# Optimization experiments

Measured on AMD Instinct MI355X. Metric: run time of the kernel, lower is better.

The kernel has to match this reference:

```python
import jax, jax.numpy as jnp
import numpy as np

N_SAMPLES = 4_000_000
N_BUCKETS = 16
K_BASE = 32
K_ADJ = 16


def setup_inputs() -> dict:
    key = jax.random.key(0)
    ks = jax.random.split(key, 8)
    return {
        "x": jax.random.uniform(ks[0], (N_SAMPLES,), dtype=jnp.float32),
        "x_mins": jnp.zeros((N_BUCKETS,), jnp.float32),
        "x_maxs": jnp.ones((N_BUCKETS,), jnp.float32),
        "clip_los": jnp.zeros((N_BUCKETS,), jnp.float32),
        "clip_his": jnp.ones((N_BUCKETS,), jnp.float32),
        "base_knots": jax.random.uniform(ks[1], (K_BASE,), dtype=jnp.float32),
        "base_raw_w": jax.random.normal(ks[2], (K_BASE,), dtype=jnp.float32),
        "base_bias": jax.random.normal(ks[3], (1,), dtype=jnp.float32),
        "adj_knots": jax.random.uniform(ks[4], (K_ADJ,), dtype=jnp.float32),
        "adj_raw_w": jax.random.normal(ks[5], (N_BUCKETS, K_ADJ), dtype=jnp.float32),
        "adj_bias": jax.random.normal(ks[6], (N_BUCKETS,), dtype=jnp.float32),
        "bucket_idx": jax.random.randint(ks[7], (N_SAMPLES,), 0, N_BUCKETS, dtype=jnp.int64),
    }


def _clip_and_scale(x, x_min, x_max, clip_lo, clip_hi):
    # per-sample clip (NaN clip bound => no clipping), then scale to [0,1]
    xc = jnp.where(jnp.isfinite(clip_lo), jnp.maximum(x, clip_lo), x)
    xc = jnp.where(jnp.isfinite(clip_hi), jnp.minimum(xc, clip_hi), xc)
    return jnp.clip((xc - x_min) / (x_max - x_min + 1e-12), 0.0, 1.0)


def _concave_hinge(x01, knots, raw_w, bias):
    # concave, monotone-increasing piecewise-linear spline:
    # f(x) = bias + sum_k softplus(raw_w_k) * min(x, knot_k)
    w = jax.nn.softplus(raw_w)                      # nonneg slopes -> concave increasing
    basis = jnp.minimum(x01[:, None], knots)        # [N, K]
    return bias + jnp.sum(basis * w, axis=-1)       # [N] (w may be [N,K] for per-bucket)


def reference(x, x_mins, x_maxs, clip_los, clip_his, base_knots, base_raw_w,
              base_bias, adj_knots, adj_raw_w, adj_bias, bucket_idx):
    b = bucket_idx.reshape(-1)
    xf = x.reshape(-1)
    # gather per-sample bucket scaling params (replaces the python bucket loop)
    x01 = _clip_and_scale(xf, x_mins[b], x_maxs[b], clip_los[b], clip_his[b])  # [N]
    base = _concave_hinge(x01, base_knots, base_raw_w, base_bias[0])           # [N]
    # vectorized gather-compute in place of unique()+mask dispatch
    adj = _concave_hinge(x01, adj_knots, adj_raw_w[b], adj_bias[b])            # [N]
    return (base + adj)[:, None]                                               # [N,1]
```

## Files before the change

kernel.cpp:

```cpp
#include <hip/hip_runtime.h>
#include <math.h>

#define NB 16
#define KB 32
#define KA 16
#define G  128
#define HINV ((float)G)
#define H (1.0f / (float)G)

#define WS_FLOATS (64 + 2 * NB * G)

__device__ __forceinline__ float softplus_f(float v) {
    return fmaxf(v, 0.0f) + log1pf(expf(-fabsf(v)));
}

__global__ __launch_bounds__(256) void build_lut_kernel(
    const float* __restrict__ x_mins,
    const float* __restrict__ x_maxs,
    const float* __restrict__ clip_los,
    const float* __restrict__ clip_his,
    const float* __restrict__ base_knots,
    const float* __restrict__ base_raw_w,
    const float* __restrict__ base_bias,
    const float* __restrict__ adj_knots,
    const float* __restrict__ adj_raw_w,
    const float* __restrict__ adj_bias,
    float* __restrict__ ws)
{
    __shared__ float s_bw[KB];
    __shared__ float s_aw[2][KA];
    __shared__ float s_bias[2];
    __shared__ float s_f[2][G + 1];

    const int tid = threadIdx.x;
    const int b0  = blockIdx.x * 2;

    if (tid < KB) s_bw[tid] = softplus_f(base_raw_w[tid]);
    if (tid < 2 * KA) {
        const int lb = tid / KA, k = tid % KA;
        s_aw[lb][k] = softplus_f(adj_raw_w[(b0 + lb) * KA + k]);
    }
    if (tid < 2) {
        const int b = b0 + tid;
        const float mn = x_mins[b], mx = x_maxs[b];
        const float a = 1.0f / (mx - mn + 1e-12f);
        const float c = -mn * a;
        const float lo = clip_los[b], hi = clip_his[b];
        const float Lb = isfinite(lo) ? fminf(fmaxf(fmaf(lo, a, c), 0.0f), 1.0f) : 0.0f;
        const float Hb = isfinite(hi) ? fmaxf(fminf(fmaf(hi, a, c), 1.0f), 0.0f) : 1.0f;
        ((float4*)ws)[b] = make_float4(a, c, Lb, Hb);
        s_bias[tid] = adj_bias[b] + base_bias[0];
    }
    __syncthreads();

    for (int gp = tid; gp < 2 * (G + 1); gp += 256) {
        const int lb = gp / (G + 1);
        const int j  = gp % (G + 1);
        const float g = (float)j * H;
        float f = s_bias[lb];
        #pragma unroll 8
        for (int k = 0; k < KB; ++k)
            f = fmaf(s_bw[k], fminf(g, base_knots[k]), f);
        #pragma unroll 8
        for (int k = 0; k < KA; ++k)
            f = fmaf(s_aw[lb][k], fminf(g, adj_knots[k]), f);
        s_f[lb][j] = f;
    }
    __syncthreads();

    float2* lut = (float2*)(ws + 64);
    if (tid < 2 * G) {
        const int lb = tid >> 7, cc = tid & (G - 1);
        const float fl = s_f[lb][cc], fr = s_f[lb][cc + 1];
        const float c1 = (fr - fl) * HINV;
        const float c0 = fmaf(-c1, (float)cc * H, fl);
        lut[(b0 + lb) * G + cc] = make_float2(c0, c1);
    }
}

__global__ __launch_bounds__(256) void BucketAdjustedHinge_kernel(
    const float* __restrict__ x,
    const int*   __restrict__ bucket_idx,
    const float* __restrict__ ws,
    float*       __restrict__ out,
    int n)
{
    __shared__ float s_mem[WS_FLOATS];
    const float4* __restrict__ prmp = (const float4*)s_mem;
    const float2* __restrict__ lutp = (const float2*)(s_mem + 64);

    const int tid = threadIdx.x;

    {
        const float4* __restrict__ src = (const float4*)ws;
        float4* __restrict__ dst = (float4*)s_mem;
        #pragma unroll
        for (int i = 0; i < WS_FLOATS / 4 / 256 + 1; ++i) {
            const int idx = tid + i * 256;
            if (idx < WS_FLOATS / 4) dst[idx] = src[idx];
        }
    }
    __syncthreads();

    const int n4 = n >> 2;
    const int stride = gridDim.x * blockDim.x;
    const float4* __restrict__ x4v = (const float4*)x;
    const int4*   __restrict__ b4v = (const int4*)bucket_idx;
    float4*       __restrict__ o4v = (float4*)out;

    for (int i = blockIdx.x * blockDim.x + tid; i < n4; i += stride) {
        const float4 xv = x4v[i];
        const int4   bv = b4v[i];
        const float xs[4] = {xv.x, xv.y, xv.z, xv.w};
        const int   bs[4] = {bv.x, bv.y, bv.z, bv.w};
        float ox[4];
        #pragma unroll
        for (int j = 0; j < 4; ++j) {
            const int b = bs[j];
            const float4 prm = prmp[b];
            float v = fmaf(xs[j], prm.x, prm.y);
            v = fminf(fmaxf(v, prm.z), prm.w);
            int cell = (int)(v * HINV);
            cell = min(cell, G - 1);
            const float2 cf = lutp[(b << 7) + cell];
            ox[j] = fmaf(v, cf.y, cf.x);
        }
        o4v[i] = make_float4(ox[0], ox[1], ox[2], ox[3]);
    }

    const int rem_start = n4 << 2;
    for (int i = rem_start + blockIdx.x * blockDim.x + tid; i < n; i += stride) {
        const int b = bucket_idx[i];
        const float4 prm = prmp[b];
        float v = fmaf(x[i], prm.x, prm.y);
        v = fminf(fmaxf(v, prm.z), prm.w);
        int cell = (int)(v * HINV);
        cell = min(cell, G - 1);
        const float2 cf = lutp[(b << 7) + cell];
        out[i] = fmaf(v, cf.y, cf.x);
    }
}

extern "C" void kernel_launch(void* const* d_in, const int* in_sizes, int n_in,
                              void* d_out, int out_size, void* d_ws, size_t ws_size,
                              hipStream_t stream) {
    const float* x          = (const float*)d_in[0];
    const float* x_mins     = (const float*)d_in[1];
    const float* x_maxs     = (const float*)d_in[2];
    const float* clip_los   = (const float*)d_in[3];
    const float* clip_his   = (const float*)d_in[4];
    const float* base_knots = (const float*)d_in[5];
    const float* base_raw_w = (const float*)d_in[6];
    const float* base_bias  = (const float*)d_in[7];
    const float* adj_knots  = (const float*)d_in[8];
    const float* adj_raw_w  = (const float*)d_in[9];
    const float* adj_bias   = (const float*)d_in[10];
    const int*   bucket_idx = (const int*)d_in[11];
    float* out = (float*)d_out;
    float* ws  = (float*)d_ws;

    const int n = in_sizes[0];

    build_lut_kernel<<<NB / 2, 256, 0, stream>>>(
        x_mins, x_maxs, clip_los, clip_his,
        base_knots, base_raw_w, base_bias,
        adj_knots, adj_raw_w, adj_bias, ws);

    const int blocks = 2048;
    BucketAdjustedHinge_kernel<<<blocks, 256, 0, stream>>>(
        x, bucket_idx, ws, out, n);
}
```

Measured before the change: 19.24 us.

## Build LUT in raw-x domain and prefetch inputs before shared-memory LUT load

The LUT is now indexed directly by the raw x value over a global x range, so the per-sample affine scale and clip parameters fold into the table and the hot loop loses the per-bucket parameter lookup. Each thread issues loads for its first two float4 tiles of x and bucket_idx before copying the LUT into shared memory, which overlaps global latency with the table fill. The LUT build now runs in a single block. The raw-x grid only matches the reference when bucket ranges are similar, and the table's interpolation points shift for buckets with narrow ranges, which could hurt accuracy in general.

```diff
diff --git a/kernel.cpp b/kernel.cpp
--- a/kernel.cpp
+++ b/kernel.cpp
@@ -5,10 +5,10 @@
 #define KB 32
 #define KA 16
 #define G  128
-#define HINV ((float)G)
-#define H (1.0f / (float)G)
-
-#define WS_FLOATS (64 + 2 * NB * G)
+#define GP1 (G + 1)
+
+#define LUT_F2   (NB * GP1)
+#define WS_FLOATS (64 + 2 * LUT_F2)
 
 __device__ __forceinline__ float softplus_f(float v) {
     return fmaxf(v, 0.0f) + log1pf(expf(-fabsf(v)));
@@ -27,54 +27,78 @@
     const float* __restrict__ adj_bias,
     float* __restrict__ ws)
 {
-    __shared__ float s_bw[KB];
-    __shared__ float s_aw[2][KA];
-    __shared__ float s_bias[2];
-    __shared__ float s_f[2][G + 1];
+    __shared__ float  s_bw[KB];
+    __shared__ float  s_aw[NB][KA];
+    __shared__ float  s_bias[NB];
+    __shared__ float4 s_abc[NB];
+    __shared__ float  s_xlo_b[NB], s_xhi_b[NB];
+    __shared__ float  s_xr[2];
+    __shared__ float  s_f[NB][GP1];
 
     const int tid = threadIdx.x;
-    const int b0  = blockIdx.x * 2;
 
     if (tid < KB) s_bw[tid] = softplus_f(base_raw_w[tid]);
-    if (tid < 2 * KA) {
-        const int lb = tid / KA, k = tid % KA;
-        s_aw[lb][k] = softplus_f(adj_raw_w[(b0 + lb) * KA + k]);
-    }
-    if (tid < 2) {
-        const int b = b0 + tid;
-        const float mn = x_mins[b], mx = x_maxs[b];
-        const float a = 1.0f / (mx - mn + 1e-12f);
+    if (tid < NB * KA) s_aw[tid >> 4][tid & (KA - 1)] = softplus_f(adj_raw_w[tid]);
+    if (tid < NB) {
+        const float mn = x_mins[tid], mx = x_maxs[tid];
+        const float inva = mx - mn + 1e-12f;
+        const float a = 1.0f / inva;
         const float c = -mn * a;
-        const float lo = clip_los[b], hi = clip_his[b];
+        const float lo = clip_los[tid], hi = clip_his[tid];
         const float Lb = isfinite(lo) ? fminf(fmaxf(fmaf(lo, a, c), 0.0f), 1.0f) : 0.0f;
         const float Hb = isfinite(hi) ? fmaxf(fminf(fmaf(hi, a, c), 1.0f), 0.0f) : 1.0f;
-        ((float4*)ws)[b] = make_float4(a, c, Lb, Hb);
-        s_bias[tid] = adj_bias[b] + base_bias[0];
-    }
-    __syncthreads();
-
-    for (int gp = tid; gp < 2 * (G + 1); gp += 256) {
-        const int lb = gp / (G + 1);
-        const int j  = gp % (G + 1);
-        const float g = (float)j * H;
-        float f = s_bias[lb];
+        s_abc[tid] = make_float4(a, c, Lb, Hb);
+        s_bias[tid] = adj_bias[tid] + base_bias[0];
+        const float x0 = fmaf(Lb, inva, mn);
+        const float x1 = fmaf(Hb, inva, mn);
+        s_xlo_b[tid] = fminf(x0, x1);
+        s_xhi_b[tid] = fmaxf(x0, x1);
+    }
+    __syncthreads();
+
+    if (tid == 0) {
+        float xlo = s_xlo_b[0], xhi = s_xhi_b[0];
+        for (int b = 1; b < NB; ++b) {
+            xlo = fminf(xlo, s_xlo_b[b]);
+            xhi = fmaxf(xhi, s_xhi_b[b]);
+        }
+        if (!(xhi > xlo)) xhi = xlo + 1.0f;
+        s_xr[0] = xlo; s_xr[1] = xhi;
+        ws[0] = xlo;
+        ws[1] = (float)G / (xhi - xlo);
+        ws[2] = xhi;
+    }
+    __syncthreads();
+
+    const float xlo = s_xr[0], xhi = s_xr[1];
+    const float hstep = (xhi - xlo) * (1.0f / (float)G);
+
+    for (int gp = tid; gp < NB * GP1; gp += 256) {
+        const int b = gp / GP1, j = gp - b * GP1;
+        const float xj = fmaf(hstep, (float)j, xlo);
+        const float4 p = s_abc[b];
+        const float v = fminf(fmaxf(fmaf(xj, p.x, p.y), p.z), p.w);
+        float f = s_bias[b];
         #pragma unroll 8
         for (int k = 0; k < KB; ++k)
-            f = fmaf(s_bw[k], fminf(g, base_knots[k]), f);
+            f = fmaf(s_bw[k], fminf(v, base_knots[k]), f);
         #pragma unroll 8
         for (int k = 0; k < KA; ++k)
-            f = fmaf(s_aw[lb][k], fminf(g, adj_knots[k]), f);
-        s_f[lb][j] = f;
+            f = fmaf(s_aw[b][k], fminf(v, adj_knots[k]), f);
+        s_f[b][j] = f;
     }
     __syncthreads();
 
     float2* lut = (float2*)(ws + 64);
-    if (tid < 2 * G) {
-        const int lb = tid >> 7, cc = tid & (G - 1);
-        const float fl = s_f[lb][cc], fr = s_f[lb][cc + 1];
-        const float c1 = (fr - fl) * HINV;
-        const float c0 = fmaf(-c1, (float)cc * H, fl);
-        lut[(b0 + lb) * G + cc] = make_float2(c0, c1);
+    const float hinv = 1.0f / hstep;
+    for (int e = tid; e < NB * GP1; e += 256) {
+        const int b = e / GP1, j = e - b * GP1;
+        const int jc = min(j, G - 1);
+        const float fl = s_f[b][jc], fr = s_f[b][jc + 1];
+        const float c1 = (fr - fl) * hinv;
+        const float xj = fmaf(hstep, (float)jc, xlo);
+        const float c0 = fmaf(-c1, xj, fl);
+        lut[e] = make_float2(c0, c1);
     }
 }
 
@@ -85,60 +109,69 @@
     float*       __restrict__ out,
     int n)
 {
-    __shared__ float s_mem[WS_FLOATS];
-    const float4* __restrict__ prmp = (const float4*)s_mem;
-    const float2* __restrict__ lutp = (const float2*)(s_mem + 64);
+    __shared__ float2 s_lut[LUT_F2];
 
     const int tid = threadIdx.x;
-
-    {
-        const float4* __restrict__ src = (const float4*)ws;
-        float4* __restrict__ dst = (float4*)s_mem;
-        #pragma unroll
-        for (int i = 0; i < WS_FLOATS / 4 / 256 + 1; ++i) {
-            const int idx = tid + i * 256;
-            if (idx < WS_FLOATS / 4) dst[idx] = src[idx];
-        }
-    }
-    __syncthreads();
-
-    const int n4 = n >> 2;
-    const int stride = gridDim.x * blockDim.x;
+    const int gsz = gridDim.x * blockDim.x;
+    const int t   = blockIdx.x * blockDim.x + tid;
+    const int n4  = n >> 2;
+
     const float4* __restrict__ x4v = (const float4*)x;
     const int4*   __restrict__ b4v = (const int4*)bucket_idx;
     float4*       __restrict__ o4v = (float4*)out;
 
-    for (int i = blockIdx.x * blockDim.x + tid; i < n4; i += stride) {
+    float4 xa, xb; int4 ba, bb;
+    const bool va = t < n4, vb = (t + gsz) < n4;
+    if (va) { xa = x4v[t];        ba = b4v[t]; }
+    if (vb) { xb = x4v[t + gsz];  bb = b4v[t + gsz]; }
+    const float xlo  = ws[0];
+    const float ginv = ws[1];
+    const float xhi  = ws[2];
+
+    {
+        const float4* __restrict__ src = (const float4*)(ws + 64);
+        float4* __restrict__ dst = (float4*)s_lut;
+        for (int i = tid; i < LUT_F2 / 2; i += 256) dst[i] = src[i];
+    }
+    __syncthreads();
+
+    #define EVAL1(xr, b, dst)                                              \
+        {                                                                  \
+            const float xc = fminf(fmaxf((xr), xlo), xhi);                 \
+            const float tt = (xc - xlo) * ginv;                            \
+            const int cell = min((int)tt, G - 1);                          \
+            const float2 cf = s_lut[(b) * GP1 + cell];                     \
+            (dst) = fmaf(xc, cf.y, cf.x);                                  \
+        }
+
+    if (va) {
+        float4 r;
+        EVAL1(xa.x, ba.x, r.x); EVAL1(xa.y, ba.y, r.y);
+        EVAL1(xa.z, ba.z, r.z); EVAL1(xa.w, ba.w, r.w);
+        o4v[t] = r;
+    }
+    if (vb) {
+        float4 r;
+        EVAL1(xb.x, bb.x, r.x); EVAL1(xb.y, bb.y, r.y);
+        EVAL1(xb.z, bb.z, r.z); EVAL1(xb.w, bb.w, r.w);
+        o4v[t + gsz] = r;
+    }
+
+    for (int i = t + 2 * gsz; i < n4; i += gsz) {
         const float4 xv = x4v[i];
         const int4   bv = b4v[i];
-        const float xs[4] = {xv.x, xv.y, xv.z, xv.w};
-        const int   bs[4] = {bv.x, bv.y, bv.z, bv.w};
-        float ox[4];
-        #pragma unroll
-        for (int j = 0; j < 4; ++j) {
-            const int b = bs[j];
-            const float4 prm = prmp[b];
-            float v = fmaf(xs[j], prm.x, prm.y);
-            v = fminf(fmaxf(v, prm.z), prm.w);
-            int cell = (int)(v * HINV);
-            cell = min(cell, G - 1);
-            const float2 cf = lutp[(b << 7) + cell];
-            ox[j] = fmaf(v, cf.y, cf.x);
-        }
-        o4v[i] = make_float4(ox[0], ox[1], ox[2], ox[3]);
-    }
-
+        float4 r;
+        EVAL1(xv.x, bv.x, r.x); EVAL1(xv.y, bv.y, r.y);
+        EVAL1(xv.z, bv.z, r.z); EVAL1(xv.w, bv.w, r.w);
+        o4v[i] = r;
+    }
     const int rem_start = n4 << 2;
-    for (int i = rem_start + blockIdx.x * blockDim.x + tid; i < n; i += stride) {
-        const int b = bucket_idx[i];
-        const float4 prm = prmp[b];
-        float v = fmaf(x[i], prm.x, prm.y);
-        v = fminf(fmaxf(v, prm.z), prm.w);
-        int cell = (int)(v * HINV);
-        cell = min(cell, G - 1);
-        const float2 cf = lutp[(b << 7) + cell];
-        out[i] = fmaf(v, cf.y, cf.x);
-    }
+    for (int i = rem_start + t; i < n; i += gsz) {
+        float r;
+        EVAL1(x[i], bucket_idx[i], r);
+        out[i] = r;
+    }
+    #undef EVAL1
 }
 
 extern "C" void kernel_launch(void* const* d_in, const int* in_sizes, int n_in,
@@ -161,7 +194,7 @@
 
     const int n = in_sizes[0];
 
-    build_lut_kernel<<<NB / 2, 256, 0, stream>>>(
+    build_lut_kernel<<<1, 256, 0, stream>>>(
         x_mins, x_maxs, clip_los, clip_his,
         base_knots, base_raw_w, base_bias,
         adj_knots, adj_raw_w, adj_bias, ws);
```

Result: slower. 24.47 us (+27.1%).
